# Kernel optimization log

Hardware: AMD Instinct MI355X
Metric: run time of the kernel (lower is better)

## Reference

```python
import jax, jax.numpy as jnp
import numpy as np

# Module configuration (from init_kwargs)
NLAT_IN, NLON_IN = 181, 360
NLAT_OUT, NLON_OUT = 361, 720
KSIZE = 3            # kernel_size of piecewise-linear basis with kernel_shape=3
CIN, COUT = 16, 16   # groups=1 -> groupsize = CIN
NNZ = 8192           # nonzeros in the precomputed psi tensor
B = 1


def setup_inputs() -> dict:
    key = jax.random.key(0)
    ks = jax.random.split(key, 6)
    x = jax.random.normal(ks[0], (B, CIN, NLAT_IN, NLON_IN), dtype=jnp.float32)
    # weight init: sqrt(1/groupsize) * basis init factors * randn
    scale = np.float32(np.sqrt(1.0 / CIN))
    weight = scale * jax.random.normal(ks[1], (COUT, CIN, KSIZE), dtype=jnp.float32)
    bias = jnp.zeros((COUT,), dtype=jnp.float32)
    # synthetic COO psi tensor (geometry-free but structurally identical)
    ker_idx = jax.random.randint(ks[2], (NNZ,), 0, KSIZE, dtype=jnp.int32)
    row_idx = jax.random.randint(ks[3], (NNZ,), 0, NLAT_IN, dtype=jnp.int32)
    col_idx = jax.random.randint(ks[4], (NNZ,), 0, NLAT_OUT * NLON_OUT, dtype=jnp.int32)
    vals = jax.random.uniform(ks[5], (NNZ,), dtype=jnp.float32) * (100.0 / NNZ)
    return {"x": x, "weight": weight, "bias": bias,
            "ker_idx": ker_idx, "row_idx": row_idx, "col_idx": col_idx, "vals": vals}


def reference(x, weight, bias, ker_idx, row_idx, col_idx, vals):
    """DISCO transpose conv on S2: channel-mix einsum, then sparse
    gather-multiply-scatter (adjoint of the longitude-shift-equivariant
    sparse contraction). col_idx encodes (out_lat, lon_offset)."""
    Bb, Cin, H, W = x.shape            # (B, C_in, nlat_in, nlon_in)
    Cout, gs, K = weight.shape
    pscale = NLON_OUT // W             # exact p-shift upsampling factor

    # 1) channel mixing with per-kernel-basis weights (groups=1)
    xw = jnp.einsum('bcxy,ock->bokxy', x, weight)   # [B, Cout, K, nlat_in, nlon_in]

    # 2) gather rows referenced by the sparse psi tensor and scale by vals
    g = xw[:, :, ker_idx, row_idx, :] * vals[None, None, :, None]  # [B, Cout, NNZ, W]

    # 3) scatter-add: each nonzero (k, tin, (tout, p)) contributes the whole
    #    longitude ring of input lat tin to output lat tout at lons (p + po*pscale)
    hi = col_idx // NLON_OUT                      # output latitude  [NNZ]
    p = col_idx % NLON_OUT                        # longitude offset [NNZ]
    lon = (p[:, None] + jnp.arange(W, dtype=p.dtype)[None, :] * pscale) % NLON_OUT  # [NNZ, W]
    flat = (hi[:, None] * NLON_OUT + lon).reshape(-1)  # [NNZ*W]

    out = jnp.zeros((Bb, Cout, NLAT_OUT * NLON_OUT), dtype=x.dtype)
    out = out.at[:, :, flat].add(g.reshape(Bb, Cout, -1))
    out = out.reshape(Bb, Cout, NLAT_OUT, NLON_OUT)
    return out + bias[None, :, None, None]
```

## Files before the change

kernel.cpp:

```cpp
#include <hip/hip_runtime.h>

#define H_IN   181
#define W_IN   360
#define NLAT   361
#define NLON   720
#define CIN    16
#define COUT   16
#define KSZ    3
#define NNZ    8192
#define HW     (H_IN * W_IN)
#define KHW    (KSZ * HW)
#define MAXB   48
#define NMIX_BLK 768
#define XW_BYTES (4 * (size_t)KHW * 16)


static __device__ __forceinline__ int rfl_i(int i) {
    return __builtin_amdgcn_readfirstlane(i);
}
static __device__ __forceinline__ float rfl_f(float f) {
    return __uint_as_float(__builtin_amdgcn_readfirstlane(__float_as_uint(f)));
}
__device__ __forceinline__ void fma4(float4& a, float v, const float4& f) {
    a.x += v * f.x; a.y += v * f.y; a.z += v * f.z; a.w += v * f.w;
}

__global__ __launch_bounds__(256) void mix_bucket_kernel(
    const float* __restrict__ x,
    const float* __restrict__ w,
    const int*   __restrict__ ker_idx,
    const int*   __restrict__ row_idx,
    const int*   __restrict__ col_idx,
    const float* __restrict__ vals,
    float4* __restrict__ xw4,
    int*   __restrict__ gcnt,
    int4*  __restrict__ gseg)
{
    const int tid = threadIdx.x;

    if (blockIdx.x >= NMIX_BLK) {
        const int ho = blockIdx.x - NMIX_BLK;
        __shared__ int   s_cnt[2];
        __shared__ int   s_b [2 * MAXB];
        __shared__ int   s_ps[2 * MAXB];
        __shared__ float s_v [2 * MAXB];

        if (tid < 2) s_cnt[tid] = 0;
        if (tid < 2 * MAXB) { s_b[tid] = 0; s_ps[tid] = 0; s_v[tid] = 0.f; }
        __syncthreads();

        const int cbase = ho * NLON;
        const int4* __restrict__ col4 = (const int4*)col_idx;
        for (int n4 = tid; n4 < NNZ / 4; n4 += 256) {
            const int4 c4 = col4[n4];
#pragma unroll
            for (int j = 0; j < 4; ++j) {
                const int c = (j == 0) ? c4.x : (j == 1) ? c4.y : (j == 2) ? c4.z : c4.w;
                const unsigned d = (unsigned)(c - cbase);
                if (d < (unsigned)NLON) {
                    const int n    = 4 * n4 + j;
                    const int pe   = (int)(d & 1u);
                    const int slot = atomicAdd(&s_cnt[pe], 1);
                    if (slot < MAXB) {
                        s_b [pe * MAXB + slot] = (ker_idx[n] * H_IN + row_idx[n]) * W_IN;
                        s_ps[pe * MAXB + slot] = (int)(d >> 1);
                        s_v [pe * MAXB + slot] = vals[n];
                    }
                }
            }
        }
        __syncthreads();
        if (tid < 2) {
            int c = s_cnt[tid] < MAXB ? s_cnt[tid] : MAXB;
            gcnt[ho * 2 + tid] = (c + 3) & ~3;
        }
        for (int i = tid; i < 2 * MAXB; i += 256) {
            gseg[ho * 2 * MAXB + i] =
                make_int4(s_b[i], s_ps[i], __float_as_int(s_v[i]), 0);
        }
        return;
    }

    const int k   = blockIdx.x >> 8;
    const int pos = (blockIdx.x & 255) * 256 + tid;

    __shared__ float sw[CIN * COUT];
    {
        const int co = tid & 15, c = tid >> 4;
        sw[tid] = w[(co * CIN + c) * KSZ + k];
    }
    __syncthreads();

    if (pos >= HW) return;

    float4 a0 = make_float4(0.f, 0.f, 0.f, 0.f), a1 = a0, a2 = a0, a3 = a0;
#pragma unroll
    for (int c = 0; c < CIN; ++c) {
        const float xv = x[c * HW + pos];
        const float4* wr = (const float4*)(sw + c * COUT);
        fma4(a0, xv, wr[0]);
        fma4(a1, xv, wr[1]);
        fma4(a2, xv, wr[2]);
        fma4(a3, xv, wr[3]);
    }

    const int e = k * HW + pos;
    xw4[0 * KHW + e] = a0;
    xw4[1 * KHW + e] = a1;
    xw4[2 * KHW + e] = a2;
    xw4[3 * KHW + e] = a3;
}

__global__ __launch_bounds__(384) void gather_kernel(
    const float4* __restrict__ xw4,
    const float* __restrict__ bias,
    const int*   __restrict__ gcnt,
    const int4*  __restrict__ gseg,
    float* __restrict__ out)
{
    const int bid   = blockIdx.x;
    const int r     = bid & 7;
    const int inner = bid >> 3;
    const int q     = r >> 1;
    const int ho    = inner * 2 + (r & 1);
    if (ho >= NLAT) return;
    const int tid = threadIdx.x;
    if (tid >= 360) return;
    const int t = tid;

    const int2 cnt2 = ((const int2*)gcnt)[ho];
    const int cntE = rfl_i(cnt2.x);
    const int cntO = rfl_i(cnt2.y);

    const float4 bq = ((const float4*)bias)[q];
    float4 accE = bq, accO = bq;
    const float4* __restrict__ slice = xw4 + (size_t)q * KHW;
    const int4*  __restrict__ seg    = gseg + ho * 2 * MAXB;

#define SEG(PE, CNT, ACC)                                                       \
    for (int e = 0; e < (CNT); e += 4) {                                        \
        const int4 s0 = seg[(PE) * MAXB + e + 0];                               \
        const int4 s1 = seg[(PE) * MAXB + e + 1];                               \
        const int4 s2 = seg[(PE) * MAXB + e + 2];                               \
        const int4 s3 = seg[(PE) * MAXB + e + 3];                               \
        const int   b0 = rfl_i(s0.x), b1 = rfl_i(s1.x);                         \
        const int   b2 = rfl_i(s2.x), b3 = rfl_i(s3.x);                         \
        const int   p0 = rfl_i(s0.y), p1 = rfl_i(s1.y);                         \
        const int   p2 = rfl_i(s2.y), p3 = rfl_i(s3.y);                         \
        const float v0 = rfl_f(__int_as_float(s0.z));                           \
        const float v1 = rfl_f(__int_as_float(s1.z));                           \
        const float v2 = rfl_f(__int_as_float(s2.z));                           \
        const float v3 = rfl_f(__int_as_float(s3.z));                           \
        int y0 = t - p0; y0 += (y0 >> 31) & 360;                                \
        int y1 = t - p1; y1 += (y1 >> 31) & 360;                                \
        int y2 = t - p2; y2 += (y2 >> 31) & 360;                                \
        int y3 = t - p3; y3 += (y3 >> 31) & 360;                                \
        const float4 f0 = slice[b0 + y0];                                       \
        const float4 f1 = slice[b1 + y1];                                       \
        const float4 f2 = slice[b2 + y2];                                       \
        const float4 f3 = slice[b3 + y3];                                       \
        fma4(ACC, v0, f0); fma4(ACC, v1, f1);                                   \
        fma4(ACC, v2, f2); fma4(ACC, v3, f3);                                   \
    }

    SEG(0, cntE, accE)
    SEG(1, cntO, accO)
#undef SEG

    const float2 rr[4] = { make_float2(accE.x, accO.x), make_float2(accE.y, accO.y),
                           make_float2(accE.z, accO.z), make_float2(accE.w, accO.w) };
#pragma unroll
    for (int j = 0; j < 4; ++j) {
        const int co = 4 * q + j;
        *(float2*)(out + ((size_t)co * NLAT + ho) * NLON + 2 * t) = rr[j];
    }
}

extern "C" void kernel_launch(void* const* d_in, const int* in_sizes, int n_in,
                              void* d_out, int out_size, void* d_ws, size_t ws_size,
                              hipStream_t stream) {
    const float* x       = (const float*)d_in[0];
    const float* weight  = (const float*)d_in[1];
    const float* bias    = (const float*)d_in[2];
    const int*   ker_idx = (const int*)d_in[3];
    const int*   row_idx = (const int*)d_in[4];
    const int*   col_idx = (const int*)d_in[5];
    const float* vals    = (const float*)d_in[6];
    float* out = (float*)d_out;

    float4* xw4  = (float4*)d_ws;
    int*    gcnt = (int*)((char*)d_ws + XW_BYTES);
    int4*   gseg = (int4*)((char*)d_ws + XW_BYTES + 4096);

    mix_bucket_kernel<<<NMIX_BLK + NLAT, 256, 0, stream>>>(
        x, weight, ker_idx, row_idx, col_idx, vals, xw4, gcnt, gseg);
    gather_kernel<<<1448, 384, 0, stream>>>(xw4, bias, gcnt, gseg, out);
}
```

Measured before the change: 98.95 us.

## Fuse mix and gather into cooperative kernel with bf16 intermediate

Merges the channel-mix/bucketing kernel and the gather kernel into one persistent cooperative kernel separated by a grid sync, with a two-launch fallback. The intermediate xw tensor is stored as bf16 instead of fp32, halving its write and gather-read traffic. The gather work unit is split into half-longitude rows with 256-thread blocks. This adds a grid-wide barrier and loses precision in the intermediate, and the persistent grid of at most 1024 blocks may limit parallelism.

```diff
diff --git a/kernel.cpp b/kernel.cpp
--- a/kernel.cpp
+++ b/kernel.cpp
@@ -1,4 +1,7 @@
 #include <hip/hip_runtime.h>
+#include <hip/hip_cooperative_groups.h>
+
+namespace cg = cooperative_groups;
 
 #define H_IN   181
 #define W_IN   360
@@ -11,10 +14,19 @@
 #define HW     (H_IN * W_IN)
 #define KHW    (KSZ * HW)
 #define MAXB   48
-#define NMIX_BLK 768
-#define XW_BYTES (4 * (size_t)KHW * 16)
-
-
+#define NUNIT  (NLAT * 8)
+#define XW_BYTES ((size_t)4 * KHW * 8)
+
+
+static __device__ __forceinline__ unsigned short f2bf(float f) {
+    unsigned int u = __float_as_uint(f);
+    u = (u + 0x7fffu + ((u >> 16) & 1u)) >> 16;
+    return (unsigned short)u;
+}
+static __device__ __forceinline__ void bf2_to_f2(unsigned int d, float& lo, float& hi) {
+    lo = __uint_as_float(d << 16);
+    hi = __uint_as_float(d & 0xffff0000u);
+}
 static __device__ __forceinline__ int rfl_i(int i) {
     return __builtin_amdgcn_readfirstlane(i);
 }
@@ -24,118 +36,128 @@
 __device__ __forceinline__ void fma4(float4& a, float v, const float4& f) {
     a.x += v * f.x; a.y += v * f.y; a.z += v * f.z; a.w += v * f.w;
 }
-
-__global__ __launch_bounds__(256) void mix_bucket_kernel(
+static __device__ __forceinline__ float4 ld_bf4(const ushort4* p) {
+    const uint2 d = *(const uint2*)p;
+    float4 f;
+    bf2_to_f2(d.x, f.x, f.y);
+    bf2_to_f2(d.y, f.z, f.w);
+    return f;
+}
+
+__global__ __launch_bounds__(256, 2) void disco_fused(
     const float* __restrict__ x,
     const float* __restrict__ w,
+    const float* __restrict__ bias,
     const int*   __restrict__ ker_idx,
     const int*   __restrict__ row_idx,
     const int*   __restrict__ col_idx,
     const float* __restrict__ vals,
-    float4* __restrict__ xw4,
-    int*   __restrict__ gcnt,
-    int4*  __restrict__ gseg)
+    ushort4*     __restrict__ xw4,
+    int*         __restrict__ gcnt,
+    int4*        __restrict__ gseg,
+    float*       __restrict__ out,
+    int phase)
 {
     const int tid = threadIdx.x;
-
-    if (blockIdx.x >= NMIX_BLK) {
-        const int ho = blockIdx.x - NMIX_BLK;
-        __shared__ int   s_cnt[2];
-        __shared__ int   s_b [2 * MAXB];
-        __shared__ int   s_ps[2 * MAXB];
-        __shared__ float s_v [2 * MAXB];
-
-        if (tid < 2) s_cnt[tid] = 0;
-        if (tid < 2 * MAXB) { s_b[tid] = 0; s_ps[tid] = 0; s_v[tid] = 0.f; }
+    const int bid = blockIdx.x;
+    const int nb  = gridDim.x;
+
+    __shared__ float swk[KSZ * CIN * COUT];
+    __shared__ int   s_cnt[2];
+    __shared__ int   s_b [2 * MAXB];
+    __shared__ int   s_ps[2 * MAXB];
+    __shared__ float s_v [2 * MAXB];
+
+    if (phase <= 1) {
+        for (int i = tid; i < KSZ * CIN * COUT; i += 256) {
+            const int k = i >> 8, rem = i & 255;
+            const int c = rem >> 4, co = rem & 15;
+            swk[i] = w[(co * CIN + c) * KSZ + k];
+        }
         __syncthreads();
 
-        const int cbase = ho * NLON;
-        const int4* __restrict__ col4 = (const int4*)col_idx;
-        for (int n4 = tid; n4 < NNZ / 4; n4 += 256) {
-            const int4 c4 = col4[n4];
+        for (int idx = bid * 256 + tid; idx < KHW; idx += nb * 256) {
+            const int k   = idx / HW;
+            const int pos = idx - k * HW;
+            float4 a0 = make_float4(0.f, 0.f, 0.f, 0.f), a1 = a0, a2 = a0, a3 = a0;
 #pragma unroll
-            for (int j = 0; j < 4; ++j) {
-                const int c = (j == 0) ? c4.x : (j == 1) ? c4.y : (j == 2) ? c4.z : c4.w;
-                const unsigned d = (unsigned)(c - cbase);
-                if (d < (unsigned)NLON) {
-                    const int n    = 4 * n4 + j;
-                    const int pe   = (int)(d & 1u);
-                    const int slot = atomicAdd(&s_cnt[pe], 1);
-                    if (slot < MAXB) {
-                        s_b [pe * MAXB + slot] = (ker_idx[n] * H_IN + row_idx[n]) * W_IN;
-                        s_ps[pe * MAXB + slot] = (int)(d >> 1);
-                        s_v [pe * MAXB + slot] = vals[n];
+            for (int c = 0; c < CIN; ++c) {
+                const float xv = x[c * HW + pos];
+                const float4* wr = (const float4*)(swk + (k * CIN + c) * COUT);
+                fma4(a0, xv, wr[0]); fma4(a1, xv, wr[1]);
+                fma4(a2, xv, wr[2]); fma4(a3, xv, wr[3]);
+            }
+            ushort4 b;
+            b.x = f2bf(a0.x); b.y = f2bf(a0.y); b.z = f2bf(a0.z); b.w = f2bf(a0.w);
+            xw4[0 * KHW + idx] = b;
+            b.x = f2bf(a1.x); b.y = f2bf(a1.y); b.z = f2bf(a1.z); b.w = f2bf(a1.w);
+            xw4[1 * KHW + idx] = b;
+            b.x = f2bf(a2.x); b.y = f2bf(a2.y); b.z = f2bf(a2.z); b.w = f2bf(a2.w);
+            xw4[2 * KHW + idx] = b;
+            b.x = f2bf(a3.x); b.y = f2bf(a3.y); b.z = f2bf(a3.z); b.w = f2bf(a3.w);
+            xw4[3 * KHW + idx] = b;
+        }
+
+        for (int ho = bid; ho < NLAT; ho += nb) {
+            if (tid < 2) s_cnt[tid] = 0;
+            for (int i = tid; i < 2 * MAXB; i += 256) {
+                s_b[i] = 0; s_ps[i] = 0; s_v[i] = 0.f;
+            }
+            __syncthreads();
+
+            const int cbase = ho * NLON;
+            const int4* __restrict__ col4 = (const int4*)col_idx;
+            for (int n4 = tid; n4 < NNZ / 4; n4 += 256) {
+                const int4 c4 = col4[n4];
+#pragma unroll
+                for (int j = 0; j < 4; ++j) {
+                    const int c = (j == 0) ? c4.x : (j == 1) ? c4.y : (j == 2) ? c4.z : c4.w;
+                    const unsigned d = (unsigned)(c - cbase);
+                    if (d < (unsigned)NLON) {
+                        const int n    = 4 * n4 + j;
+                        const int pe   = (int)(d & 1u);
+                        const int slot = atomicAdd(&s_cnt[pe], 1);
+                        if (slot < MAXB) {
+                            s_b [pe * MAXB + slot] = (ker_idx[n] * H_IN + row_idx[n]) * W_IN;
+                            s_ps[pe * MAXB + slot] = (int)(d >> 1);
+                            s_v [pe * MAXB + slot] = vals[n];
+                        }
                     }
                 }
             }
-        }
-        __syncthreads();
-        if (tid < 2) {
-            int c = s_cnt[tid] < MAXB ? s_cnt[tid] : MAXB;
-            gcnt[ho * 2 + tid] = (c + 3) & ~3;
-        }
-        for (int i = tid; i < 2 * MAXB; i += 256) {
-            gseg[ho * 2 * MAXB + i] =
-                make_int4(s_b[i], s_ps[i], __float_as_int(s_v[i]), 0);
-        }
-        return;
-    }
-
-    const int k   = blockIdx.x >> 8;
-    const int pos = (blockIdx.x & 255) * 256 + tid;
-
-    __shared__ float sw[CIN * COUT];
-    {
-        const int co = tid & 15, c = tid >> 4;
-        sw[tid] = w[(co * CIN + c) * KSZ + k];
-    }
-    __syncthreads();
-
-    if (pos >= HW) return;
-
-    float4 a0 = make_float4(0.f, 0.f, 0.f, 0.f), a1 = a0, a2 = a0, a3 = a0;
-#pragma unroll
-    for (int c = 0; c < CIN; ++c) {
-        const float xv = x[c * HW + pos];
-        const float4* wr = (const float4*)(sw + c * COUT);
-        fma4(a0, xv, wr[0]);
-        fma4(a1, xv, wr[1]);
-        fma4(a2, xv, wr[2]);
-        fma4(a3, xv, wr[3]);
-    }
-
-    const int e = k * HW + pos;
-    xw4[0 * KHW + e] = a0;
-    xw4[1 * KHW + e] = a1;
-    xw4[2 * KHW + e] = a2;
-    xw4[3 * KHW + e] = a3;
-}
-
-__global__ __launch_bounds__(384) void gather_kernel(
-    const float4* __restrict__ xw4,
-    const float* __restrict__ bias,
-    const int*   __restrict__ gcnt,
-    const int4*  __restrict__ gseg,
-    float* __restrict__ out)
-{
-    const int bid   = blockIdx.x;
-    const int r     = bid & 7;
-    const int inner = bid >> 3;
-    const int q     = r >> 1;
-    const int ho    = inner * 2 + (r & 1);
-    if (ho >= NLAT) return;
-    const int tid = threadIdx.x;
-    if (tid >= 360) return;
-    const int t = tid;
-
-    const int2 cnt2 = ((const int2*)gcnt)[ho];
-    const int cntE = rfl_i(cnt2.x);
-    const int cntO = rfl_i(cnt2.y);
-
-    const float4 bq = ((const float4*)bias)[q];
-    float4 accE = bq, accO = bq;
-    const float4* __restrict__ slice = xw4 + (size_t)q * KHW;
-    const int4*  __restrict__ seg    = gseg + ho * 2 * MAXB;
+            __syncthreads();
+            if (tid < 2) {
+                int c = s_cnt[tid] < MAXB ? s_cnt[tid] : MAXB;
+                gcnt[ho * 2 + tid] = (c + 3) & ~3;
+            }
+            for (int i = tid; i < 2 * MAXB; i += 256)
+                gseg[ho * 2 * MAXB + i] =
+                    make_int4(s_b[i], s_ps[i], __float_as_int(s_v[i]), 0);
+            __syncthreads();
+        }
+    }
+
+    if (phase == 0) {
+        __threadfence();
+        cg::this_grid().sync();
+    }
+
+    if (phase != 1) {
+        for (int u = bid; u < NUNIT; u += nb) {
+            const int ho   = u >> 3;
+            const int q    = (u >> 1) & 3;
+            const int half = u & 1;
+
+            const int2 cnt2 = ((const int2*)gcnt)[ho];
+            const int cntE = rfl_i(cnt2.x);
+            const int cntO = rfl_i(cnt2.y);
+
+            if (tid < 180) {
+                const int lonIdx = half * 180 + tid;
+                const float4 bq = ((const float4*)bias)[q];
+                float4 accE = bq, accO = bq;
+                const ushort4* __restrict__ slice = xw4 + (size_t)q * KHW;
+                const int4*   __restrict__ seg    = gseg + ho * 2 * MAXB;
 
 #define SEG(PE, CNT, ACC)                                                       \
     for (int e = 0; e < (CNT); e += 4) {                                        \
@@ -151,28 +173,31 @@
         const float v1 = rfl_f(__int_as_float(s1.z));                           \
         const float v2 = rfl_f(__int_as_float(s2.z));                           \
         const float v3 = rfl_f(__int_as_float(s3.z));                           \
-        int y0 = t - p0; y0 += (y0 >> 31) & 360;                                \
-        int y1 = t - p1; y1 += (y1 >> 31) & 360;                                \
-        int y2 = t - p2; y2 += (y2 >> 31) & 360;                                \
-        int y3 = t - p3; y3 += (y3 >> 31) & 360;                                \
-        const float4 f0 = slice[b0 + y0];                                       \
-        const float4 f1 = slice[b1 + y1];                                       \
-        const float4 f2 = slice[b2 + y2];                                       \
-        const float4 f3 = slice[b3 + y3];                                       \
+        int y0 = lonIdx - p0; y0 += (y0 >> 31) & 360;                           \
+        int y1 = lonIdx - p1; y1 += (y1 >> 31) & 360;                           \
+        int y2 = lonIdx - p2; y2 += (y2 >> 31) & 360;                           \
+        int y3 = lonIdx - p3; y3 += (y3 >> 31) & 360;                           \
+        const float4 f0 = ld_bf4(slice + b0 + y0);                              \
+        const float4 f1 = ld_bf4(slice + b1 + y1);                              \
+        const float4 f2 = ld_bf4(slice + b2 + y2);                              \
+        const float4 f3 = ld_bf4(slice + b3 + y3);                              \
         fma4(ACC, v0, f0); fma4(ACC, v1, f1);                                   \
         fma4(ACC, v2, f2); fma4(ACC, v3, f3);                                   \
     }
-
-    SEG(0, cntE, accE)
-    SEG(1, cntO, accO)
+                SEG(0, cntE, accE)
+                SEG(1, cntO, accO)
 #undef SEG
 
-    const float2 rr[4] = { make_float2(accE.x, accO.x), make_float2(accE.y, accO.y),
-                           make_float2(accE.z, accO.z), make_float2(accE.w, accO.w) };
+                const float2 rr[4] = {
+                    make_float2(accE.x, accO.x), make_float2(accE.y, accO.y),
+                    make_float2(accE.z, accO.z), make_float2(accE.w, accO.w) };
 #pragma unroll
-    for (int j = 0; j < 4; ++j) {
-        const int co = 4 * q + j;
-        *(float2*)(out + ((size_t)co * NLAT + ho) * NLON + 2 * t) = rr[j];
+                for (int j = 0; j < 4; ++j) {
+                    const int co = 4 * q + j;
+                    *(float2*)(out + ((size_t)co * NLAT + ho) * NLON + 2 * lonIdx) = rr[j];
+                }
+            }
+        }
     }
 }
 
@@ -188,11 +213,38 @@
     const float* vals    = (const float*)d_in[6];
     float* out = (float*)d_out;
 
-    float4* xw4  = (float4*)d_ws;
-    int*    gcnt = (int*)((char*)d_ws + XW_BYTES);
-    int4*   gseg = (int4*)((char*)d_ws + XW_BYTES + 4096);
-
-    mix_bucket_kernel<<<NMIX_BLK + NLAT, 256, 0, stream>>>(
-        x, weight, ker_idx, row_idx, col_idx, vals, xw4, gcnt, gseg);
-    gather_kernel<<<1448, 384, 0, stream>>>(xw4, bias, gcnt, gseg, out);
-}
+    ushort4* xw4  = (ushort4*)d_ws;
+    int*     gcnt = (int*)((char*)d_ws + XW_BYTES);
+    int4*    gseg = (int4*)((char*)d_ws + XW_BYTES + 4096);
+
+    static int coop_grid = -2;
+    if (coop_grid == -2) {
+        int occ = 0;
+        if (hipOccupancyMaxActiveBlocksPerMultiprocessor(&occ, disco_fused, 256, 0)
+                == hipSuccess && occ > 0) {
+            long g = (long)occ * 256;
+            coop_grid = (int)(g > 1024 ? 1024 : g);
+        } else {
+            coop_grid = -1;
+        }
+    }
+
+    if (coop_grid > 0) {
+        int phase = 0;
+        void* args[] = {
+            (void*)&x, (void*)&weight, (void*)&bias,
+            (void*)&ker_idx, (void*)&row_idx, (void*)&col_idx, (void*)&vals,
+            (void*)&xw4, (void*)&gcnt, (void*)&gseg, (void*)&out, (void*)&phase };
+        hipError_t e = hipLaunchCooperativeKernel(
+            disco_fused, dim3(coop_grid), dim3(256), args, 0, stream);
+        if (e == hipSuccess) return;
+        coop_grid = -1;
+    }
+
+    disco_fused<<<1024, 256, 0, stream>>>(
+        x, weight, bias, ker_idx, row_idx, col_idx, vals,
+        xw4, gcnt, gseg, out, 1);
+    disco_fused<<<1444, 256, 0, stream>>>(
+        x, weight, bias, ker_idx, row_idx, col_idx, vals,
+        xw4, gcnt, gseg, out, 2);
+}
```

New measurement: 290.8 us. 194% more time.

## Store mixed intermediate as bf16 and gather eight channels per block

Applied to the files above, without the earlier changes.

The channel-mixed intermediate xw is now stored as packed bf16 (8 output channels per 16-byte load) instead of fp32 float4, halving the workspace written by the mix kernel and read by the gather kernel. The gather grid is restructured so each block covers 8 output channels of one output latitude (722 blocks instead of 1448), and the per-latitude segment list is staged in shared memory. This reduces memory traffic on the bandwidth-bound gather, at the cost of bf16 rounding error in the intermediate, which may exceed tolerance.

```diff
diff --git a/kernel.cpp b/kernel.cpp
--- a/kernel.cpp
+++ b/kernel.cpp
@@ -12,9 +12,21 @@
 #define KHW    (KSZ * HW)
 #define MAXB   48
 #define NMIX_BLK 768
-#define XW_BYTES (4 * (size_t)KHW * 16)
-
-
+#define XW_BYTES ((size_t)2 * KHW * 16)
+
+
+static __device__ __forceinline__ unsigned short f2bf(float f) {
+    unsigned int u = __float_as_uint(f);
+    u = (u + 0x7fffu + ((u >> 16) & 1u)) >> 16;
+    return (unsigned short)u;
+}
+static __device__ __forceinline__ unsigned int pack2(float a, float b) {
+    return (unsigned int)f2bf(a) | ((unsigned int)f2bf(b) << 16);
+}
+static __device__ __forceinline__ void bf2_to_f2(unsigned int d, float& lo, float& hi) {
+    lo = __uint_as_float(d << 16);
+    hi = __uint_as_float(d & 0xffff0000u);
+}
 static __device__ __forceinline__ int rfl_i(int i) {
     return __builtin_amdgcn_readfirstlane(i);
 }
@@ -23,6 +35,13 @@
 }
 __device__ __forceinline__ void fma4(float4& a, float v, const float4& f) {
     a.x += v * f.x; a.y += v * f.y; a.z += v * f.z; a.w += v * f.w;
+}
+static __device__ __forceinline__ void fma8(float4& aL, float4& aH, float v, uint4 d) {
+    float lo, hi;
+    bf2_to_f2(d.x, lo, hi); aL.x += v * lo; aL.y += v * hi;
+    bf2_to_f2(d.y, lo, hi); aL.z += v * lo; aL.w += v * hi;
+    bf2_to_f2(d.z, lo, hi); aH.x += v * lo; aH.y += v * hi;
+    bf2_to_f2(d.w, lo, hi); aH.z += v * lo; aH.w += v * hi;
 }
 
 __global__ __launch_bounds__(256) void mix_bucket_kernel(
@@ -32,7 +51,7 @@
     const int*   __restrict__ row_idx,
     const int*   __restrict__ col_idx,
     const float* __restrict__ vals,
-    float4* __restrict__ xw4,
+    uint4* __restrict__ xw8,
     int*   __restrict__ gcnt,
     int4*  __restrict__ gseg)
 {
@@ -74,10 +93,9 @@
             int c = s_cnt[tid] < MAXB ? s_cnt[tid] : MAXB;
             gcnt[ho * 2 + tid] = (c + 3) & ~3;
         }
-        for (int i = tid; i < 2 * MAXB; i += 256) {
+        for (int i = tid; i < 2 * MAXB; i += 256)
             gseg[ho * 2 * MAXB + i] =
                 make_int4(s_b[i], s_ps[i], __float_as_int(s_v[i]), 0);
-        }
         return;
     }
 
@@ -98,51 +116,54 @@
     for (int c = 0; c < CIN; ++c) {
         const float xv = x[c * HW + pos];
         const float4* wr = (const float4*)(sw + c * COUT);
-        fma4(a0, xv, wr[0]);
-        fma4(a1, xv, wr[1]);
-        fma4(a2, xv, wr[2]);
-        fma4(a3, xv, wr[3]);
+        fma4(a0, xv, wr[0]); fma4(a1, xv, wr[1]);
+        fma4(a2, xv, wr[2]); fma4(a3, xv, wr[3]);
     }
 
     const int e = k * HW + pos;
-    xw4[0 * KHW + e] = a0;
-    xw4[1 * KHW + e] = a1;
-    xw4[2 * KHW + e] = a2;
-    xw4[3 * KHW + e] = a3;
+    uint4 u;
+    u.x = pack2(a0.x, a0.y); u.y = pack2(a0.z, a0.w);
+    u.z = pack2(a1.x, a1.y); u.w = pack2(a1.z, a1.w);
+    xw8[0 * KHW + e] = u;
+    u.x = pack2(a2.x, a2.y); u.y = pack2(a2.z, a2.w);
+    u.z = pack2(a3.x, a3.y); u.w = pack2(a3.z, a3.w);
+    xw8[1 * KHW + e] = u;
 }
 
 __global__ __launch_bounds__(384) void gather_kernel(
-    const float4* __restrict__ xw4,
+    const uint4* __restrict__ xw8,
     const float* __restrict__ bias,
     const int*   __restrict__ gcnt,
     const int4*  __restrict__ gseg,
     float* __restrict__ out)
 {
-    const int bid   = blockIdx.x;
-    const int r     = bid & 7;
-    const int inner = bid >> 3;
-    const int q     = r >> 1;
-    const int ho    = inner * 2 + (r & 1);
-    if (ho >= NLAT) return;
+    const int bid = blockIdx.x;
+    const int h   = bid & 1;
+    const int ho  = bid >> 1;
     const int tid = threadIdx.x;
-    if (tid >= 360) return;
-    const int t = tid;
+
+    __shared__ int4 s_seg[2 * MAXB];
+    if (tid < 2 * MAXB) s_seg[tid] = gseg[ho * 2 * MAXB + tid];
+    __syncthreads();
 
     const int2 cnt2 = ((const int2*)gcnt)[ho];
     const int cntE = rfl_i(cnt2.x);
     const int cntO = rfl_i(cnt2.y);
 
-    const float4 bq = ((const float4*)bias)[q];
-    float4 accE = bq, accO = bq;
-    const float4* __restrict__ slice = xw4 + (size_t)q * KHW;
-    const int4*  __restrict__ seg    = gseg + ho * 2 * MAXB;
-
-#define SEG(PE, CNT, ACC)                                                       \
+    if (tid >= 360) return;
+    const int t = tid;
+
+    const float4 bL = ((const float4*)bias)[2 * h];
+    const float4 bH = ((const float4*)bias)[2 * h + 1];
+    float4 accEL = bL, accEH = bH, accOL = bL, accOH = bH;
+    const uint4* __restrict__ slice = xw8 + (size_t)h * KHW;
+
+#define SEG(PE, CNT, ACCL, ACCH)                                                \
     for (int e = 0; e < (CNT); e += 4) {                                        \
-        const int4 s0 = seg[(PE) * MAXB + e + 0];                               \
-        const int4 s1 = seg[(PE) * MAXB + e + 1];                               \
-        const int4 s2 = seg[(PE) * MAXB + e + 2];                               \
-        const int4 s3 = seg[(PE) * MAXB + e + 3];                               \
+        const int4 s0 = s_seg[(PE) * MAXB + e + 0];                             \
+        const int4 s1 = s_seg[(PE) * MAXB + e + 1];                             \
+        const int4 s2 = s_seg[(PE) * MAXB + e + 2];                             \
+        const int4 s3 = s_seg[(PE) * MAXB + e + 3];                             \
         const int   b0 = rfl_i(s0.x), b1 = rfl_i(s1.x);                         \
         const int   b2 = rfl_i(s2.x), b3 = rfl_i(s3.x);                         \
         const int   p0 = rfl_i(s0.y), p1 = rfl_i(s1.y);                         \
@@ -155,23 +176,26 @@
         int y1 = t - p1; y1 += (y1 >> 31) & 360;                                \
         int y2 = t - p2; y2 += (y2 >> 31) & 360;                                \
         int y3 = t - p3; y3 += (y3 >> 31) & 360;                                \
-        const float4 f0 = slice[b0 + y0];                                       \
-        const float4 f1 = slice[b1 + y1];                                       \
-        const float4 f2 = slice[b2 + y2];                                       \
-        const float4 f3 = slice[b3 + y3];                                       \
-        fma4(ACC, v0, f0); fma4(ACC, v1, f1);                                   \
-        fma4(ACC, v2, f2); fma4(ACC, v3, f3);                                   \
-    }
-
-    SEG(0, cntE, accE)
-    SEG(1, cntO, accO)
+        const uint4 f0 = slice[b0 + y0];                                        \
+        const uint4 f1 = slice[b1 + y1];                                        \
+        const uint4 f2 = slice[b2 + y2];                                        \
+        const uint4 f3 = slice[b3 + y3];                                        \
+        fma8(ACCL, ACCH, v0, f0); fma8(ACCL, ACCH, v1, f1);                     \
+        fma8(ACCL, ACCH, v2, f2); fma8(ACCL, ACCH, v3, f3);                     \
+    }
+
+    SEG(0, cntE, accEL, accEH)
+    SEG(1, cntO, accOL, accOH)
 #undef SEG
 
-    const float2 rr[4] = { make_float2(accE.x, accO.x), make_float2(accE.y, accO.y),
-                           make_float2(accE.z, accO.z), make_float2(accE.w, accO.w) };
+    const float2 rr[8] = {
+        make_float2(accEL.x, accOL.x), make_float2(accEL.y, accOL.y),
+        make_float2(accEL.z, accOL.z), make_float2(accEL.w, accOL.w),
+        make_float2(accEH.x, accOH.x), make_float2(accEH.y, accOH.y),
+        make_float2(accEH.z, accOH.z), make_float2(accEH.w, accOH.w) };
 #pragma unroll
-    for (int j = 0; j < 4; ++j) {
-        const int co = 4 * q + j;
+    for (int j = 0; j < 8; ++j) {
+        const int co = 8 * h + j;
         *(float2*)(out + ((size_t)co * NLAT + ho) * NLON + 2 * t) = rr[j];
     }
 }
@@ -188,11 +212,11 @@
     const float* vals    = (const float*)d_in[6];
     float* out = (float*)d_out;
 
-    float4* xw4  = (float4*)d_ws;
-    int*    gcnt = (int*)((char*)d_ws + XW_BYTES);
-    int4*   gseg = (int4*)((char*)d_ws + XW_BYTES + 4096);
+    uint4* xw8  = (uint4*)d_ws;
+    int*   gcnt = (int*)((char*)d_ws + XW_BYTES);
+    int4*  gseg = (int4*)((char*)d_ws + XW_BYTES + 4096);
 
     mix_bucket_kernel<<<NMIX_BLK + NLAT, 256, 0, stream>>>(
-        x, weight, ker_idx, row_idx, col_idx, vals, xw4, gcnt, gseg);
-    gather_kernel<<<1448, 384, 0, stream>>>(xw4, bias, gcnt, gseg, out);
-}
+        x, weight, ker_idx, row_idx, col_idx, vals, xw8, gcnt, gseg);
+    gather_kernel<<<NLAT * 2, 384, 0, stream>>>(xw8, bias, gcnt, gseg, out);
+}
```

After: 93.14 us. -5.9%, faster.
